# Kernel optimization log

Hardware: AMD Instinct MI355X
Metric: run time of the kernel (lower is better)

Reference implementation:

```python
import jax, jax.numpy as jnp
import numpy as np

N, E, D = 50000, 300000, 64
ETYPES = ['temporal', 'assigned_to', 'com', 'tin', 'win', 'sin', 'take_time', 'use_time']


def setup_inputs():
    key = jax.random.key(0)
    ks = iter(jax.random.split(key, 80))

    def nrm(shape, s=1.0):
        return jax.random.normal(next(ks), shape, dtype=jnp.float32) * s

    inp = {}
    inp['feat_task'] = nrm((N, D))
    inp['feat_worker'] = nrm((N, D))
    inp['feat_state'] = nrm((N, D))
    for et in ETYPES:
        inp['src_' + et] = jax.random.randint(next(ks), (E,), 0, N, dtype=jnp.int32)
        inp['dst_' + et] = jax.random.randint(next(ks), (E,), 0, N, dtype=jnp.int32)
    inp['w_temporal'] = jax.random.uniform(next(ks), (E, 1), dtype=jnp.float32)
    inp['t_take_time'] = jax.random.uniform(next(ks), (E, 1), dtype=jnp.float32)
    inp['t_use_time'] = jax.random.uniform(next(ks), (E, 1), dtype=jnp.float32)
    for et in ETYPES:
        inp['W_' + et] = nrm((D, D), 0.05)
        inp['b_' + et] = nrm((D,), 0.05)
    for nm in ['edge_fc', 'edge_fc_ttr', 'edge_fc_rut']:
        inp[nm + '_W'] = nrm((D, 1), 0.05)
        inp[nm + '_b'] = nrm((D,), 0.05)
    inp['attn_W'] = nrm((1, 3 * D), 0.05)
    inp['attn_ttr_W'] = nrm((1, 3 * D), 0.05)
    inp['attn_rut_W'] = nrm((1, 3 * D), 0.05)
    inp['attn_assigned_W'] = nrm((1, 2 * D), 0.05)
    inp['attn_com_W'] = nrm((1, 2 * D), 0.05)
    inp['attn_tin_W'] = nrm((1, 2 * D), 0.05)
    inp['attn_rin_W'] = nrm((1, 2 * D), 0.05)
    return inp


def _seg_softmax_sum(e, msg, dst, n):
    # numerically stable segment softmax over each dst node's incoming edges,
    # followed by the alpha-weighted scatter-sum (DGL reduce_func).
    m = jax.ops.segment_max(e, dst, num_segments=n)        # [n,1]
    ex = jnp.exp(e - m[dst])                               # [E,1]
    den = jax.ops.segment_sum(ex, dst, num_segments=n)     # [n,1]
    return jax.ops.segment_sum((ex / den[dst]) * msg, dst, num_segments=n)


def _gat(Wh_s, Wh_d, src, dst, aW, n, zij=None):
    # e = leaky_relu(attn_fc(concat(z_src, z_dst[, zij]))); the concat is never
    # materialized -- attn weight is split into per-block dot products.
    d = Wh_s.shape[1]
    zs = Wh_s[src]
    e = zs @ aW[0, :d] + Wh_d[dst] @ aW[0, d:2 * d]
    if zij is not None:
        e = e + zij @ aW[0, 2 * d:]
        msg = zs + zij   # message_func: src Wh + edge embedding
    else:
        msg = zs
    e = jax.nn.leaky_relu(e, 0.2)[:, None]
    return _seg_softmax_sum(e, msg, dst, n)


def _forward(feat_task, feat_worker, feat_state, w_temporal, t_take_time, t_use_time,
             W_temporal, b_temporal, W_assigned_to, b_assigned_to, W_com, b_com,
             W_tin, b_tin, W_win, b_win, W_sin, b_sin, W_take_time, b_take_time,
             W_use_time, b_use_time, edge_fc_W, edge_fc_b, edge_fc_ttr_W, edge_fc_ttr_b,
             edge_fc_rut_W, edge_fc_rut_b, attn_W, attn_assigned_W, attn_com_W,
             attn_tin_W, attn_rin_W, attn_ttr_W, attn_rut_W,
             src_temporal, dst_temporal, src_assigned_to, dst_assigned_to,
             src_com, dst_com, src_tin, dst_tin, src_win, dst_win,
             src_sin, dst_sin, src_take_time, dst_take_time, src_use_time, dst_use_time):
    n_task, n_worker, n_state = feat_task.shape[0], feat_worker.shape[0], feat_state.shape[0]
    # Equation (1): per-etype linear projection of source node features
    Wh_temporal = feat_task @ W_temporal.T + b_temporal
    Wh_assigned = feat_task @ W_assigned_to.T + b_assigned_to
    Wh_com = feat_worker @ W_com.T + b_com
    Wh_tin = feat_task @ W_tin.T + b_tin
    Wh_win = feat_worker @ W_win.T + b_win
    Wh_sin = feat_state @ W_sin.T + b_sin
    Wh_ttr = feat_task @ W_take_time.T + b_take_time
    Wh_rut = feat_worker @ W_use_time.T + b_use_time
    # per-edge scalar feature -> d-dim embedding
    zij_t = w_temporal @ edge_fc_W.T + edge_fc_b
    zij_ttr = t_take_time @ edge_fc_ttr_W.T + edge_fc_ttr_b
    zij_rut = t_use_time @ edge_fc_rut_W.T + edge_fc_rut_b
    # Equations (2)-(4): per-etype attention + segment softmax + scatter-sum
    h_temporal = _gat(Wh_temporal, Wh_temporal, src_temporal, dst_temporal, attn_W, n_task, zij_t)
    h_assigned = _gat(Wh_assigned, Wh_com, src_assigned_to, dst_assigned_to, attn_assigned_W, n_worker)
    h_com = _gat(Wh_com, Wh_com, src_com, dst_com, attn_com_W, n_worker)
    h_tin = _gat(Wh_tin, Wh_sin, src_tin, dst_tin, attn_tin_W, n_state)
    h_win = _gat(Wh_win, Wh_sin, src_win, dst_win, attn_rin_W, n_state)
    h_sin = jax.ops.segment_sum(Wh_sin[src_sin], dst_sin, num_segments=n_state)  # copy_src + sum
    h_ttr = _gat(Wh_ttr, Wh_com, src_take_time, dst_take_time, attn_ttr_W, n_worker, zij_ttr)
    h_rut = _gat(Wh_rut, Wh_temporal, src_use_time, dst_use_time, attn_rut_W, n_task, zij_rut)
    # multi_update_all cross-type 'sum', then ReLU
    h_task = jax.nn.relu(h_temporal + h_rut)
    h_worker = jax.nn.relu(h_assigned + h_com + h_ttr)
    h_state = jax.nn.relu(h_tin + h_win + h_sin)
    return jnp.stack([h_task, h_worker, h_state])  # [3, N, D]


def reference(feat_task, feat_worker, feat_state,
              src_temporal, dst_temporal, src_assigned_to, dst_assigned_to,
              src_com, dst_com, src_tin, dst_tin, src_win, dst_win,
              src_sin, dst_sin, src_take_time, dst_take_time, src_use_time, dst_use_time,
              w_temporal, t_take_time, t_use_time,
              W_temporal, b_temporal, W_assigned_to, b_assigned_to, W_com, b_com,
              W_tin, b_tin, W_win, b_win, W_sin, b_sin, W_take_time, b_take_time,
              W_use_time, b_use_time, edge_fc_W, edge_fc_b, edge_fc_ttr_W, edge_fc_ttr_b,
              edge_fc_rut_W, edge_fc_rut_b, attn_W, attn_ttr_W, attn_rut_W,
              attn_assigned_W, attn_com_W, attn_tin_W, attn_rin_W):
    return _forward(feat_task, feat_worker, feat_state, w_temporal, t_take_time, t_use_time,
                    W_temporal, b_temporal, W_assigned_to, b_assigned_to, W_com, b_com,
                    W_tin, b_tin, W_win, b_win, W_sin, b_sin, W_take_time, b_take_time,
                    W_use_time, b_use_time, edge_fc_W, edge_fc_b, edge_fc_ttr_W, edge_fc_ttr_b,
                    edge_fc_rut_W, edge_fc_rut_b, attn_W, attn_assigned_W, attn_com_W,
                    attn_tin_W, attn_rin_W, attn_ttr_W, attn_rut_W,
                    src_temporal, dst_temporal, src_assigned_to, dst_assigned_to,
                    src_com, dst_com, src_tin, dst_tin, src_win, dst_win,
                    src_sin, dst_sin, src_take_time, dst_take_time, src_use_time, dst_use_time)
```

## Files before the change

kernel.cpp:

```cpp
#include <hip/hip_runtime.h>
#include <math.h>

#define NN 50000
#define EE 300000
#define NG 8
#define NTOT (NG * NN)
#define NBKT 782
#define BCAP 3584
#define TILE 1024
#define NBLKE ((EE + TILE - 1) / TILE)

typedef unsigned short u16;
typedef unsigned int u32;
typedef short bf16x8 __attribute__((ext_vector_type(8)));
typedef float f32x16 __attribute__((ext_vector_type(16)));

__device__ __forceinline__ float b2f(u16 u) { return __uint_as_float(((u32)u) << 16); }
__device__ __forceinline__ u16 f2b(float f) {
    u32 x = __float_as_uint(f);
    u32 lsb = (x >> 16) & 1u;
    return (u16)((x + 0x7fffu + lsb) >> 16);
}

__global__ void HeteroGATLayer_14259291423309_kernel() {}

struct SetupP {
    int* gcur;
    const float* attn[3]; const float* fcW[3]; const float* fcb[3];
    float* consts;
};

__global__ __launch_bounds__(256) void k_setup(SetupP p) {
    const int i = blockIdx.x * 256 + threadIdx.x;
    if (i < NBKT) p.gcur[i] = 0;
    if (blockIdx.x == 3) {
        const int z = threadIdx.x >> 6, lane = threadIdx.x & 63;
        if (z < 3) {
            float a2 = p.attn[z][128 + lane];
            float x = p.fcW[z][lane] * a2;
            float y = p.fcb[z][lane] * a2;
            #pragma unroll
            for (int off = 32; off; off >>= 1) {
                x += __shfl_down(x, off);
                y += __shfl_down(y, off);
            }
            if (lane == 0) {
                const int co[3] = {0, 10, 12};
                p.consts[co[z]] = x;
                p.consts[co[z] + 1] = y;
            }
        }
    }
}

struct ProjP {
    const float* feat[3];
    const float* W[8]; const float* b[8];
    u16* wh;
    int ntile[3]; int tiles[3][4];
    int nvec[8];
    const float* avec[8][4];
    float* dvec[8][4];
};

__global__ __launch_bounds__(256) void k_proj(ProjP p) {
    __shared__ u16 sA[64 * 64];
    __shared__ u16 sW[64 * 64];
    __shared__ u16 sC[64 * 66];
    const int f = blockIdx.y;
    const int tid = threadIdx.x;
    const int row0 = blockIdx.x * 64;
    const float* feat = p.feat[f];

    #pragma unroll
    for (int q = 0; q < 4; ++q) {
        int idx = q * 256 + tid;
        int r = idx >> 4;
        int c4 = (idx & 15) * 4;
        int gr = row0 + r;
        if (gr >= NN) gr = NN - 1;
        float4 fv = *(const float4*)(feat + (size_t)gr * 64 + c4);
        *(ushort4*)&sA[r * 64 + c4] = make_ushort4(f2b(fv.x), f2b(fv.y), f2b(fv.z), f2b(fv.w));
    }

    const int wv = tid >> 6, lane = tid & 63;
    const int mrow = (wv & 1) * 32, ncol = (wv >> 1) * 32;
    const int half = lane >> 5, l31 = lane & 31;
    const int nt = p.ntile[f];

    for (int ti = 0; ti < nt; ++ti) {
        const int t = p.tiles[f][ti];
        const float* W = p.W[t];
        #pragma unroll
        for (int q = 0; q < 4; ++q) {
            int idx = q * 256 + tid;
            int r = idx >> 4;
            int c4 = (idx & 15) * 4;
            float4 wv4 = *(const float4*)(W + r * 64 + c4);
            *(ushort4*)&sW[r * 64 + c4] = make_ushort4(f2b(wv4.x), f2b(wv4.y), f2b(wv4.z), f2b(wv4.w));
        }
        __syncthreads();

        f32x16 acc;
        #pragma unroll
        for (int i = 0; i < 16; ++i) acc[i] = 0.0f;
        #pragma unroll
        for (int k0 = 0; k0 < 64; k0 += 16) {
            bf16x8 af = *(const bf16x8*)&sA[(mrow + l31) * 64 + k0 + half * 8];
            bf16x8 bf = *(const bf16x8*)&sW[(ncol + l31) * 64 + k0 + half * 8];
            acc = __builtin_amdgcn_mfma_f32_32x32x16_bf16(af, bf, acc, 0, 0, 0);
        }

        float bb = p.b[t][ncol + l31];
        u16* whp = p.wh + (size_t)t * NN * 64;
        #pragma unroll
        for (int reg = 0; reg < 16; ++reg) {
            int rowD = (reg & 3) + 8 * (reg >> 2) + 4 * half;
            int gr = row0 + mrow + rowD;
            u16 c16 = f2b(acc[reg] + bb);
            if (gr < NN) whp[(size_t)gr * 64 + ncol + l31] = c16;
            sC[(mrow + rowD) * 66 + ncol + l31] = c16;
        }
        __syncthreads();

        const int r = tid & 63, j = tid >> 6;
        if (j < p.nvec[t]) {
            const float* av = p.avec[t][j];
            float s = 0.f;
            #pragma unroll
            for (int c = 0; c < 64; c += 4) {
                ushort4 cv = *(const ushort4*)&sC[r * 66 + c];
                float4 a4 = *(const float4*)(av + c);
                s += b2f(cv.x) * a4.x + b2f(cv.y) * a4.y + b2f(cv.z) * a4.z + b2f(cv.w) * a4.w;
            }
            int gr = row0 + r;
            if (gr < NN) p.dvec[t][j][gr] = s;
        }
    }
}

struct BinAP {
    const int* src[8]; const int* dst[8]; const float* w[8];
    const float* el[8]; const float* er[8];
    const float* consts;
    int whoff[8];
    int* gcur; int4* bkt;
};

__global__ __launch_bounds__(256) void k_binA(BinAP p) {
    __shared__ int hist[128];
    const int g = blockIdx.y;
    const int b0 = (g * NN) >> 9;
    const int tid = threadIdx.x;
    const int e = blockIdx.x * TILE + tid * 4;
    if (tid < 128) hist[tid] = 0;

    const bool hw = p.w[g] != 0;
    float c1 = 0.f, c0 = 0.f;
    if (g < 7 && hw) { c1 = p.consts[2 * g]; c0 = p.consts[2 * g + 1]; }
    const int wo = p.whoff[g];

    int sr[4], bl[4], low[4];
    float sc[4], pw[4];
    const bool valid = e < EE;
    if (valid) {
        int4 s4 = *(const int4*)(p.src[g] + e);
        int4 d4 = *(const int4*)(p.dst[g] + e);
        float4 w4 = make_float4(0.f, 0.f, 0.f, 0.f);
        if (hw) w4 = *(const float4*)(p.w[g] + e);
        int ss[4] = {s4.x, s4.y, s4.z, s4.w};
        int dd[4] = {d4.x, d4.y, d4.z, d4.w};
        float ww[4] = {w4.x, w4.y, w4.z, w4.w};
        #pragma unroll
        for (int q = 0; q < 4; ++q) {
            int key = g * NN + dd[q];
            bl[q] = (key >> 9) - b0;
            low[q] = key & 511;
            sr[q] = wo + (ss[q] << 7);
            float scv = 1.0f, pwv = 0.0f;
            if (g < 7) {
                scv = p.el[g][ss[q]] + p.er[g][dd[q]];
                if (hw) scv += c1 * ww[q] + c0;
                scv = scv > 0.f ? scv : 0.2f * scv;
                scv = __expf(scv);
                if (hw) pwv = scv * ww[q];
            }
            sc[q] = scv; pw[q] = pwv;
        }
    }
    __syncthreads();
    if (valid) {
        #pragma unroll
        for (int q = 0; q < 4; ++q) atomicAdd(&hist[bl[q]], 1);
    }
    __syncthreads();
    if (tid < 128) {
        int c = hist[tid];
        hist[tid] = c ? atomicAdd(&p.gcur[b0 + tid], c) : 0;
    }
    __syncthreads();
    if (valid) {
        #pragma unroll
        for (int q = 0; q < 4; ++q) {
            int pos = atomicAdd(&hist[bl[q]], 1);
            int4 v;
            v.x = sr[q];
            v.y = __float_as_int(sc[q]);
            v.z = __float_as_int(pw[q]);
            v.w = low[q];
            p.bkt[(size_t)(b0 + bl[q]) * BCAP + pos] = v;
        }
    }
}

__global__ __launch_bounds__(512) void k_binB(const int* __restrict__ gcur,
                                              const int4* __restrict__ bkt,
                                              int2* __restrict__ csr,
                                              int4* __restrict__ rowdeg) {
    __shared__ int2 st2[BCAP];
    __shared__ float st3[BCAP];
    __shared__ int hist[512];
    __shared__ int scn[512];
    __shared__ int wsum[8];
    const int b = blockIdx.x;
    const int tid = threadIdx.x;
    int count = gcur[b];
    if (count > BCAP) count = BCAP;
    hist[tid] = 0;
    __syncthreads();
    const int4* src = bkt + (size_t)b * BCAP;
    for (int i = tid; i < count; i += 512) atomicAdd(&hist[src[i].w], 1);
    __syncthreads();
    int h = hist[tid];
    const int lane = tid & 63, wvi = tid >> 6;
    int incl = h;
    #pragma unroll
    for (int off = 1; off < 64; off <<= 1) {
        int t = __shfl_up(incl, off);
        if (lane >= off) incl += t;
    }
    if (lane == 63) wsum[wvi] = incl;
    __syncthreads();
    int wb = 0;
    #pragma unroll
    for (int w = 0; w < 8; ++w)
        if (w < wvi) wb += wsum[w];
    const int excl = wb + incl - h;
    scn[tid] = excl;
    __syncthreads();
    for (int i = tid; i < count; i += 512) {
        int4 v = src[i];
        int pos = atomicAdd(&scn[v.w], 1);
        st2[pos] = make_int2(v.x, v.y);
        st3[pos] = __int_as_float(v.z);
    }
    __syncthreads();
    float den = 0.f, sw = 0.f;
    for (int j = 0; j < h; ++j) {
        den += __int_as_float(st2[excl + j].y);
        sw += st3[excl + j];
    }
    const int gkey = b * 512 + tid;
    if (gkey < NTOT) {
        float inv = (gkey >= 7 * NN) ? 1.0f : ((h > 0 && den > 0.f) ? 1.0f / den : 0.f);
        u32 beg = (u32)(b * BCAP + excl);
        rowdeg[gkey] = make_int4((int)((beg << 10) | (u32)h),
                                 __float_as_int(inv), __float_as_int(sw * inv), 0);
    }
    for (int i = tid; i < count; i += 512) csr[(size_t)b * BCAP + i] = st2[i];
}

struct GathP {
    int gidx[3][3]; int hasfc[3][3];
    const float* fcW[3][3]; const float* fcb[3][3];
};

#define GSTEP4(t, sp)                                                              \
    {                                                                              \
        int2 e0 = sp[k], e1 = sp[k + 1], e2 = sp[k + 2], e3 = sp[k + 3];           \
        u32 w0 = *(const u32*)(whA + (u32)(e0.x + dby));                           \
        u32 w1 = *(const u32*)(whA + (u32)(e1.x + dby));                           \
        u32 w2 = *(const u32*)(whA + (u32)(e2.x + dby));                           \
        u32 w3 = *(const u32*)(whA + (u32)(e3.x + dby));                           \
        acc0[t] += __int_as_float(e0.y) * b2f((u16)w0);                            \
        acc1[t] += __int_as_float(e0.y) * b2f((u16)(w0 >> 16));                    \
        acc0[t] += __int_as_float(e1.y) * b2f((u16)w1);                            \
        acc1[t] += __int_as_float(e1.y) * b2f((u16)(w1 >> 16));                    \
        acc0[t] += __int_as_float(e2.y) * b2f((u16)w2);                            \
        acc1[t] += __int_as_float(e2.y) * b2f((u16)(w2 >> 16));                    \
        acc0[t] += __int_as_float(e3.y) * b2f((u16)w3);                            \
        acc1[t] += __int_as_float(e3.y) * b2f((u16)(w3 >> 16));                    \
    }

__global__ __launch_bounds__(256) void k_gather(GathP p,
        const int4* __restrict__ rowdeg, const int2* __restrict__ csr,
        const char* __restrict__ whA, float* __restrict__ out) {
    __shared__ int2 sSeg[4][3][2][64];
    const int tg = blockIdx.y;
    const int wv = threadIdx.x >> 6, lane = threadIdx.x & 63;
    const int half = lane >> 5, c = lane & 31;
    const int i = blockIdx.x * 8 + wv * 2 + half;
    const int dby = c * 4;
    const int ng = (tg == 0) ? 2 : 3;

    int lenv[3]; u32 begv[3]; float invv[3], swv[3];
    #pragma unroll
    for (int t = 0; t < 3; ++t) {
        lenv[t] = 0; begv[t] = 0; invv[t] = 0.f; swv[t] = 0.f;
        if (t < ng) {
            int4 rv = rowdeg[p.gidx[tg][t] * NN + i];
            lenv[t] = rv.x & 1023;
            begv[t] = ((u32)rv.x) >> 10;
            invv[t] = __int_as_float(rv.y);
            swv[t] = __int_as_float(rv.z);
        }
    }
    int lenA[3], lenB[3], lmax[3]; u32 begA[3], begB[3];
    #pragma unroll
    for (int t = 0; t < 3; ++t) {
        lenA[t] = __builtin_amdgcn_readlane(lenv[t], 0);
        lenB[t] = __builtin_amdgcn_readlane(lenv[t], 32);
        begA[t] = (u32)__builtin_amdgcn_readlane((int)begv[t], 0);
        begB[t] = (u32)__builtin_amdgcn_readlane((int)begv[t], 32);
        lmax[t] = lenA[t] > lenB[t] ? lenA[t] : lenB[t];
    }
    int kall = lmax[0] > lmax[1] ? lmax[0] : lmax[1];
    kall = kall > lmax[2] ? kall : lmax[2];

    float acc0[3] = {0.f, 0.f, 0.f}, acc1[3] = {0.f, 0.f, 0.f};
    for (int cb = 0; cb < kall; cb += 64) {
        #pragma unroll
        for (int t = 0; t < 3; ++t) {
            if (cb < lmax[t]) {
                int2 vA = (lane < lenA[t] - cb) ? csr[begA[t] + cb + lane] : make_int2(0, 0);
                sSeg[wv][t][0][lane] = vA;
                int2 vB = (lane < lenB[t] - cb) ? csr[begB[t] + cb + lane] : make_int2(0, 0);
                sSeg[wv][t][1][lane] = vB;
            }
        }
        const int2* s0 = sSeg[wv][0][half];
        const int2* s1 = sSeg[wv][1][half];
        const int2* s2 = sSeg[wv][2][half];
        int l0 = lmax[0] - cb, l1 = lmax[1] - cb, l2 = lmax[2] - cb;
        if (l0 > 64) l0 = 64;
        if (l1 > 64) l1 = 64;
        if (l2 > 64) l2 = 64;
        int cmax = l0 > l1 ? l0 : l1;
        cmax = cmax > l2 ? cmax : l2;
        for (int k = 0; k < cmax; k += 4) {
            if (k < l0) GSTEP4(0, s0)
            if (k < l1) GSTEP4(1, s1)
            if (k < l2) GSTEP4(2, s2)
        }
    }

    float tot0 = 0.f, tot1 = 0.f;
    #pragma unroll
    for (int t = 0; t < 3; ++t) {
        tot0 += acc0[t] * invv[t];
        tot1 += acc1[t] * invv[t];
        if (p.hasfc[tg][t]) {
            bool he = lenv[t] > 0;
            float2 fw = *(const float2*)(p.fcW[tg][t] + 2 * c);
            float2 fb = *(const float2*)(p.fcb[tg][t] + 2 * c);
            tot0 += he ? (fw.x * swv[t] + fb.x) : 0.f;
            tot1 += he ? (fw.y * swv[t] + fb.y) : 0.f;
        }
    }
    float2 o;
    o.x = tot0 > 0.f ? tot0 : 0.f;
    o.y = tot1 > 0.f ? tot1 : 0.f;
    *(float2*)(out + ((size_t)tg * NN + i) * 64 + 2 * c) = o;
}

extern "C" void kernel_launch(void* const* d_in, const int* in_sizes, int n_in,
                              void* d_out, int out_size, void* d_ws, size_t ws_size,
                              hipStream_t stream) {
    (void)in_sizes; (void)n_in; (void)out_size; (void)ws_size;
    const float* feats[3] = {(const float*)d_in[0], (const float*)d_in[1], (const float*)d_in[2]};
    const int* srcs[8];
    const int* dsts[8];
    for (int t = 0; t < 8; ++t) {
        srcs[t] = (const int*)d_in[3 + 2 * t];
        dsts[t] = (const int*)d_in[4 + 2 * t];
    }
    const float* ew0 = (const float*)d_in[19];
    const float* ew1 = (const float*)d_in[20];
    const float* ew2 = (const float*)d_in[21];
    const float* Wm[8];
    const float* bm[8];
    for (int t = 0; t < 8; ++t) {
        Wm[t] = (const float*)d_in[22 + 2 * t];
        bm[t] = (const float*)d_in[23 + 2 * t];
    }
    const float* fcW0 = (const float*)d_in[38];
    const float* fcb0 = (const float*)d_in[39];
    const float* fcW1 = (const float*)d_in[40];
    const float* fcb1 = (const float*)d_in[41];
    const float* fcW2 = (const float*)d_in[42];
    const float* fcb2 = (const float*)d_in[43];
    const float* attn_W          = (const float*)d_in[44];
    const float* attn_ttr_W      = (const float*)d_in[45];
    const float* attn_rut_W      = (const float*)d_in[46];
    const float* attn_assigned_W = (const float*)d_in[47];
    const float* attn_com_W      = (const float*)d_in[48];
    const float* attn_tin_W      = (const float*)d_in[49];
    const float* attn_rin_W      = (const float*)d_in[50];

    u16* Wh = (u16*)d_ws;
    char* b0 = (char*)d_ws + (size_t)8 * NN * 64 * sizeof(u16);
    float* el     = (float*)b0;
    float* er     = el + (size_t)7 * NN;
    float* consts = er + (size_t)7 * NN;
    int* gcur     = (int*)(consts + 16);
    int4* rowdeg4 = (int4*)(((size_t)(gcur + NBKT) + 15) & ~(size_t)15);
    int4* bkt     = rowdeg4 + NTOT;
    int2* csr     = (int2*)(bkt + (size_t)NBKT * BCAP);

    int g_et[8]   = {0, 1, 2, 3, 4, 6, 7, 5};
    int g_sidx[8] = {0, 1, 2, 3, 4, 6, 7, 5};
    const float* g_w[8] = {ew0, 0, 0, 0, 0, ew1, ew2, 0};

    {
        SetupP sp;
        sp.gcur = gcur;
        sp.attn[0] = attn_W;     sp.fcW[0] = fcW0; sp.fcb[0] = fcb0;
        sp.attn[1] = attn_ttr_W; sp.fcW[1] = fcW1; sp.fcb[1] = fcb1;
        sp.attn[2] = attn_rut_W; sp.fcW[2] = fcW2; sp.fcb[2] = fcb2;
        sp.consts = consts;
        k_setup<<<4, 256, 0, stream>>>(sp);
    }

    {
        ProjP pp;
        pp.feat[0] = feats[0]; pp.feat[1] = feats[1]; pp.feat[2] = feats[2];
        for (int t = 0; t < 8; ++t) { pp.W[t] = Wm[t]; pp.b[t] = bm[t]; }
        pp.wh = Wh;
        pp.ntile[0] = 4; pp.tiles[0][0] = 0; pp.tiles[0][1] = 1; pp.tiles[0][2] = 3; pp.tiles[0][3] = 6;
        pp.ntile[1] = 3; pp.tiles[1][0] = 2; pp.tiles[1][1] = 4; pp.tiles[1][2] = 7; pp.tiles[1][3] = 0;
        pp.ntile[2] = 1; pp.tiles[2][0] = 5; pp.tiles[2][1] = 0; pp.tiles[2][2] = 0; pp.tiles[2][3] = 0;
        for (int t = 0; t < 8; ++t) {
            pp.nvec[t] = 0;
            for (int j = 0; j < 4; ++j) { pp.avec[t][j] = 0; pp.dvec[t][j] = 0; }
        }
        auto setv = [&](int t, int j, const float* a, float* dv) { pp.avec[t][j] = a; pp.dvec[t][j] = dv; };
        pp.nvec[0] = 3; setv(0, 0, attn_W, el);           setv(0, 1, attn_W + 64, er);
                        setv(0, 2, attn_rut_W + 64, er + 6 * NN);
        pp.nvec[1] = 1; setv(1, 0, attn_assigned_W, el + 1 * NN);
        pp.nvec[2] = 4; setv(2, 0, attn_com_W, el + 2 * NN); setv(2, 1, attn_assigned_W + 64, er + 1 * NN);
                        setv(2, 2, attn_com_W + 64, er + 2 * NN); setv(2, 3, attn_ttr_W + 64, er + 5 * NN);
        pp.nvec[3] = 1; setv(3, 0, attn_tin_W, el + 3 * NN);
        pp.nvec[4] = 1; setv(4, 0, attn_rin_W, el + 4 * NN);
        pp.nvec[5] = 2; setv(5, 0, attn_tin_W + 64, er + 3 * NN); setv(5, 1, attn_rin_W + 64, er + 4 * NN);
        pp.nvec[6] = 1; setv(6, 0, attn_ttr_W, el + 5 * NN);
        pp.nvec[7] = 1; setv(7, 0, attn_rut_W, el + 6 * NN);
        k_proj<<<dim3(782, 3), 256, 0, stream>>>(pp);
    }

    {
        BinAP bp;
        for (int g = 0; g < 8; ++g) {
            bp.src[g] = srcs[g_et[g]];
            bp.dst[g] = dsts[g_et[g]];
            bp.w[g] = g_w[g];
            bp.el[g] = (g < 7) ? el + (size_t)g * NN : 0;
            bp.er[g] = (g < 7) ? er + (size_t)g * NN : 0;
            bp.whoff[g] = g_sidx[g] * NN * 128;
        }
        bp.consts = consts;
        bp.gcur = gcur;
        bp.bkt = bkt;
        k_binA<<<dim3(NBLKE, 8), 256, 0, stream>>>(bp);
    }
    k_binB<<<NBKT, 512, 0, stream>>>(gcur, bkt, csr, rowdeg4);

    {
        GathP gp;
        gp.gidx[0][0] = 0; gp.hasfc[0][0] = 1; gp.fcW[0][0] = fcW0; gp.fcb[0][0] = fcb0;
        gp.gidx[0][1] = 6; gp.hasfc[0][1] = 1; gp.fcW[0][1] = fcW2; gp.fcb[0][1] = fcb2;
        gp.gidx[0][2] = 0; gp.hasfc[0][2] = 0; gp.fcW[0][2] = fcW0; gp.fcb[0][2] = fcb0;
        gp.gidx[1][0] = 1; gp.hasfc[1][0] = 0; gp.fcW[1][0] = fcW0; gp.fcb[1][0] = fcb0;
        gp.gidx[1][1] = 2; gp.hasfc[1][1] = 0; gp.fcW[1][1] = fcW0; gp.fcb[1][1] = fcb0;
        gp.gidx[1][2] = 5; gp.hasfc[1][2] = 1; gp.fcW[1][2] = fcW1; gp.fcb[1][2] = fcb1;
        gp.gidx[2][0] = 3; gp.hasfc[2][0] = 0; gp.fcW[2][0] = fcW0; gp.fcb[2][0] = fcb0;
        gp.gidx[2][1] = 4; gp.hasfc[2][1] = 0; gp.fcW[2][1] = fcW0; gp.fcb[2][1] = fcb0;
        gp.gidx[2][2] = 7; gp.hasfc[2][2] = 0; gp.fcW[2][2] = fcW0; gp.fcb[2][2] = fcb0;
        k_gather<<<dim3(NN / 8, 3), 256, 0, stream>>>(gp, rowdeg4, csr,
                                                      (const char*)Wh, (float*)d_out);
    }
}
```

Baseline: 345.9 us.

## Fuse bucket sort and gather into per-node-block kernel with all types bucketed together

Edges of all eight relation types are now bucketed by destination node block (64 nodes × 8 types per bucket) in one binning launch, instead of one bucket range per type. A single fused kernel then sorts each bucket in shared memory, normalizes the softmax weights in place, and directly gathers the projected features and writes outputs for all three node types. This removes the separate CSR and rowdeg write-out, the extra kernel launch, and the reread of CSR from global memory. In exchange, bucket capacity per block must hold all types' edges, and each block's gather now loops over 64 nodes with a load-imbalanced inner loop.

```diff
diff --git a/kernel.cpp b/kernel.cpp
--- a/kernel.cpp
+++ b/kernel.cpp
@@ -4,7 +4,6 @@
 #define NN 50000
 #define EE 300000
 #define NG 8
-#define NTOT (NG * NN)
 #define NBKT 782
 #define BCAP 3584
 #define TILE 1024
@@ -45,7 +44,7 @@
                 y += __shfl_down(y, off);
             }
             if (lane == 0) {
-                const int co[3] = {0, 10, 12};
+                const int co[3] = {0, 8, 2};
                 p.consts[co[z]] = x;
                 p.consts[co[z] + 1] = y;
             }
@@ -147,80 +146,98 @@
     int* gcur; int4* bkt;
 };
 
-__global__ __launch_bounds__(256) void k_binA(BinAP p) {
-    __shared__ int hist[128];
-    const int g = blockIdx.y;
-    const int b0 = (g * NN) >> 9;
+__global__ __launch_bounds__(512) void k_binA(BinAP p) {
+    __shared__ int hist[784];
     const int tid = threadIdx.x;
-    const int e = blockIdx.x * TILE + tid * 4;
-    if (tid < 128) hist[tid] = 0;
-
-    const bool hw = p.w[g] != 0;
-    float c1 = 0.f, c0 = 0.f;
-    if (g < 7 && hw) { c1 = p.consts[2 * g]; c0 = p.consts[2 * g + 1]; }
-    const int wo = p.whoff[g];
-
-    int sr[4], bl[4], low[4];
-    float sc[4], pw[4];
+    const int e = blockIdx.x * TILE + tid * 2;
+    for (int i = tid; i < 784; i += 512) hist[i] = 0;
     const bool valid = e < EE;
-    if (valid) {
-        int4 s4 = *(const int4*)(p.src[g] + e);
-        int4 d4 = *(const int4*)(p.dst[g] + e);
-        float4 w4 = make_float4(0.f, 0.f, 0.f, 0.f);
-        if (hw) w4 = *(const float4*)(p.w[g] + e);
-        int ss[4] = {s4.x, s4.y, s4.z, s4.w};
-        int dd[4] = {d4.x, d4.y, d4.z, d4.w};
-        float ww[4] = {w4.x, w4.y, w4.z, w4.w};
+    int d0[8], d1[8];
+    __syncthreads();
+    #pragma unroll
+    for (int g = 0; g < 8; ++g) {
+        int2 dv = valid ? *(const int2*)(p.dst[g] + e) : make_int2(0, 0);
+        d0[g] = dv.x; d1[g] = dv.y;
+        if (valid) {
+            atomicAdd(&hist[dv.x >> 6], 1);
+            atomicAdd(&hist[dv.y >> 6], 1);
+        }
+    }
+    __syncthreads();
+    for (int b = tid; b < NBKT; b += 512) {
+        int c = hist[b];
+        hist[b] = c ? atomicAdd(&p.gcur[b], c) : 0;
+    }
+    __syncthreads();
+    #pragma unroll
+    for (int g = 0; g < 8; ++g) {
+        if (!valid) continue;
+        int2 sv = *(const int2*)(p.src[g] + e);
+        const float* wp = p.w[g];
+        const bool hw = wp != 0;
+        float2 wv = hw ? *(const float2*)(wp + e) : make_float2(0.f, 0.f);
+        float c1 = 0.f, c0 = 0.f;
+        if (g < 7 && hw) { c1 = p.consts[2 * g]; c0 = p.consts[2 * g + 1]; }
+        const int wo = p.whoff[g];
+        int ss[2] = {sv.x, sv.y};
+        int dd[2] = {d0[g], d1[g]};
+        float ww[2] = {wv.x, wv.y};
         #pragma unroll
-        for (int q = 0; q < 4; ++q) {
-            int key = g * NN + dd[q];
-            bl[q] = (key >> 9) - b0;
-            low[q] = key & 511;
-            sr[q] = wo + (ss[q] << 7);
-            float scv = 1.0f, pwv = 0.0f;
+        for (int q = 0; q < 2; ++q) {
+            float sc = 1.0f, pw = 0.0f;
             if (g < 7) {
-                scv = p.el[g][ss[q]] + p.er[g][dd[q]];
-                if (hw) scv += c1 * ww[q] + c0;
-                scv = scv > 0.f ? scv : 0.2f * scv;
-                scv = __expf(scv);
-                if (hw) pwv = scv * ww[q];
+                sc = p.el[g][ss[q]] + p.er[g][dd[q]];
+                if (hw) sc += c1 * ww[q] + c0;
+                sc = sc > 0.f ? sc : 0.2f * sc;
+                sc = __expf(sc);
+                if (hw) pw = sc * ww[q];
             }
-            sc[q] = scv; pw[q] = pwv;
-        }
-    }
-    __syncthreads();
-    if (valid) {
-        #pragma unroll
-        for (int q = 0; q < 4; ++q) atomicAdd(&hist[bl[q]], 1);
-    }
-    __syncthreads();
-    if (tid < 128) {
-        int c = hist[tid];
-        hist[tid] = c ? atomicAdd(&p.gcur[b0 + tid], c) : 0;
-    }
-    __syncthreads();
-    if (valid) {
-        #pragma unroll
-        for (int q = 0; q < 4; ++q) {
-            int pos = atomicAdd(&hist[bl[q]], 1);
+            int bkt_i = dd[q] >> 6;
+            int pos = atomicAdd(&hist[bkt_i], 1);
             int4 v;
-            v.x = sr[q];
-            v.y = __float_as_int(sc[q]);
-            v.z = __float_as_int(pw[q]);
-            v.w = low[q];
-            p.bkt[(size_t)(b0 + bl[q]) * BCAP + pos] = v;
-        }
-    }
-}
-
-__global__ __launch_bounds__(512) void k_binB(const int* __restrict__ gcur,
-                                              const int4* __restrict__ bkt,
-                                              int2* __restrict__ csr,
-                                              int4* __restrict__ rowdeg) {
-    __shared__ int2 st2[BCAP];
+            v.x = wo + (ss[q] << 7);
+            v.y = __float_as_int(sc);
+            v.z = __float_as_int(pw);
+            v.w = ((dd[q] & 63) << 3) | g;
+            p.bkt[(size_t)bkt_i * BCAP + pos] = v;
+        }
+    }
+}
+
+struct BgP {
+    const float* fcW[3]; const float* fcb[3];
+};
+
+#define BGSTEP4(t, baseV, lenV)                                                    \
+    {                                                                              \
+        int2 e0 = st2[baseV + k], e1 = st2[baseV + k + 1];                         \
+        int2 e2 = st2[baseV + k + 2], e3 = st2[baseV + k + 3];                     \
+        int o0 = (k < lenV) ? e0.x : 0;                                            \
+        int o1 = (k + 1 < lenV) ? e1.x : 0;                                        \
+        int o2 = (k + 2 < lenV) ? e2.x : 0;                                        \
+        int o3 = (k + 3 < lenV) ? e3.x : 0;                                        \
+        float f0 = (k < lenV) ? __int_as_float(e0.y) : 0.f;                        \
+        float f1 = (k + 1 < lenV) ? __int_as_float(e1.y) : 0.f;                    \
+        float f2 = (k + 2 < lenV) ? __int_as_float(e2.y) : 0.f;                    \
+        float f3 = (k + 3 < lenV) ? __int_as_float(e3.y) : 0.f;                    \
+        u32 w0 = *(const u32*)(whA + (u32)(o0 + dby));                             \
+        u32 w1 = *(const u32*)(whA + (u32)(o1 + dby));                             \
+        u32 w2 = *(const u32*)(whA + (u32)(o2 + dby));                             \
+        u32 w3 = *(const u32*)(whA + (u32)(o3 + dby));                             \
+        a0[t] += f0 * b2f((u16)w0); a1[t] += f0 * b2f((u16)(w0 >> 16));            \
+        a0[t] += f1 * b2f((u16)w1); a1[t] += f1 * b2f((u16)(w1 >> 16));            \
+        a0[t] += f2 * b2f((u16)w2); a1[t] += f2 * b2f((u16)(w2 >> 16));            \
+        a0[t] += f3 * b2f((u16)w3); a1[t] += f3 * b2f((u16)(w3 >> 16));            \
+    }
+
+__global__ __launch_bounds__(512) void k_bg(BgP p, const int* __restrict__ gcur,
+        const int4* __restrict__ bkt, const char* __restrict__ whA,
+        float* __restrict__ out) {
+    __shared__ int2 st2[BCAP + 128];
     __shared__ float st3[BCAP];
     __shared__ int hist[512];
     __shared__ int scn[512];
+    __shared__ float sSw[512];
     __shared__ int wsum[8];
     const int b = blockIdx.x;
     const int tid = threadIdx.x;
@@ -260,117 +277,71 @@
         den += __int_as_float(st2[excl + j].y);
         sw += st3[excl + j];
     }
-    const int gkey = b * 512 + tid;
-    if (gkey < NTOT) {
-        float inv = (gkey >= 7 * NN) ? 1.0f : ((h > 0 && den > 0.f) ? 1.0f / den : 0.f);
-        u32 beg = (u32)(b * BCAP + excl);
-        rowdeg[gkey] = make_int4((int)((beg << 10) | (u32)h),
-                                 __float_as_int(inv), __float_as_int(sw * inv), 0);
-    }
-    for (int i = tid; i < count; i += 512) csr[(size_t)b * BCAP + i] = st2[i];
-}
-
-struct GathP {
-    int gidx[3][3]; int hasfc[3][3];
-    const float* fcW[3][3]; const float* fcb[3][3];
-};
-
-#define GSTEP4(t, sp)                                                              \
-    {                                                                              \
-        int2 e0 = sp[k], e1 = sp[k + 1], e2 = sp[k + 2], e3 = sp[k + 3];           \
-        u32 w0 = *(const u32*)(whA + (u32)(e0.x + dby));                           \
-        u32 w1 = *(const u32*)(whA + (u32)(e1.x + dby));                           \
-        u32 w2 = *(const u32*)(whA + (u32)(e2.x + dby));                           \
-        u32 w3 = *(const u32*)(whA + (u32)(e3.x + dby));                           \
-        acc0[t] += __int_as_float(e0.y) * b2f((u16)w0);                            \
-        acc1[t] += __int_as_float(e0.y) * b2f((u16)(w0 >> 16));                    \
-        acc0[t] += __int_as_float(e1.y) * b2f((u16)w1);                            \
-        acc1[t] += __int_as_float(e1.y) * b2f((u16)(w1 >> 16));                    \
-        acc0[t] += __int_as_float(e2.y) * b2f((u16)w2);                            \
-        acc1[t] += __int_as_float(e2.y) * b2f((u16)(w2 >> 16));                    \
-        acc0[t] += __int_as_float(e3.y) * b2f((u16)w3);                            \
-        acc1[t] += __int_as_float(e3.y) * b2f((u16)(w3 >> 16));                    \
-    }
-
-__global__ __launch_bounds__(256) void k_gather(GathP p,
-        const int4* __restrict__ rowdeg, const int2* __restrict__ csr,
-        const char* __restrict__ whA, float* __restrict__ out) {
-    __shared__ int2 sSeg[4][3][2][64];
-    const int tg = blockIdx.y;
-    const int wv = threadIdx.x >> 6, lane = threadIdx.x & 63;
+    const int gk = tid & 7;
+    float inv = (gk == 7) ? 1.0f : ((h > 0 && den > 0.f) ? 1.0f / den : 0.f);
+    sSw[tid] = sw * inv;
+    for (int j = 0; j < h; ++j)
+        st2[excl + j].y = __float_as_int(__int_as_float(st2[excl + j].y) * inv);
+    __syncthreads();
     const int half = lane >> 5, c = lane & 31;
-    const int i = blockIdx.x * 8 + wv * 2 + half;
     const int dby = c * 4;
-    const int ng = (tg == 0) ? 2 : 3;
-
-    int lenv[3]; u32 begv[3]; float invv[3], swv[3];
-    #pragma unroll
-    for (int t = 0; t < 3; ++t) {
-        lenv[t] = 0; begv[t] = 0; invv[t] = 0.f; swv[t] = 0.f;
-        if (t < ng) {
-            int4 rv = rowdeg[p.gidx[tg][t] * NN + i];
-            lenv[t] = rv.x & 1023;
-            begv[t] = ((u32)rv.x) >> 10;
-            invv[t] = __int_as_float(rv.y);
-            swv[t] = __int_as_float(rv.z);
-        }
-    }
-    int lenA[3], lenB[3], lmax[3]; u32 begA[3], begB[3];
-    #pragma unroll
-    for (int t = 0; t < 3; ++t) {
-        lenA[t] = __builtin_amdgcn_readlane(lenv[t], 0);
-        lenB[t] = __builtin_amdgcn_readlane(lenv[t], 32);
-        begA[t] = (u32)__builtin_amdgcn_readlane((int)begv[t], 0);
-        begB[t] = (u32)__builtin_amdgcn_readlane((int)begv[t], 32);
-        lmax[t] = lenA[t] > lenB[t] ? lenA[t] : lenB[t];
-    }
-    int kall = lmax[0] > lmax[1] ? lmax[0] : lmax[1];
-    kall = kall > lmax[2] ? kall : lmax[2];
-
-    float acc0[3] = {0.f, 0.f, 0.f}, acc1[3] = {0.f, 0.f, 0.f};
-    for (int cb = 0; cb < kall; cb += 64) {
-        #pragma unroll
-        for (int t = 0; t < 3; ++t) {
-            if (cb < lmax[t]) {
-                int2 vA = (lane < lenA[t] - cb) ? csr[begA[t] + cb + lane] : make_int2(0, 0);
-                sSeg[wv][t][0][lane] = vA;
-                int2 vB = (lane < lenB[t] - cb) ? csr[begB[t] + cb + lane] : make_int2(0, 0);
-                sSeg[wv][t][1][lane] = vB;
-            }
-        }
-        const int2* s0 = sSeg[wv][0][half];
-        const int2* s1 = sSeg[wv][1][half];
-        const int2* s2 = sSeg[wv][2][half];
-        int l0 = lmax[0] - cb, l1 = lmax[1] - cb, l2 = lmax[2] - cb;
-        if (l0 > 64) l0 = 64;
-        if (l1 > 64) l1 = 64;
-        if (l2 > 64) l2 = 64;
-        int cmax = l0 > l1 ? l0 : l1;
-        cmax = cmax > l2 ? cmax : l2;
-        for (int k = 0; k < cmax; k += 4) {
-            if (k < l0) GSTEP4(0, s0)
-            if (k < l1) GSTEP4(1, s1)
-            if (k < l2) GSTEP4(2, s2)
-        }
-    }
-
-    float tot0 = 0.f, tot1 = 0.f;
-    #pragma unroll
-    for (int t = 0; t < 3; ++t) {
-        tot0 += acc0[t] * invv[t];
-        tot1 += acc1[t] * invv[t];
-        if (p.hasfc[tg][t]) {
-            bool he = lenv[t] > 0;
-            float2 fw = *(const float2*)(p.fcW[tg][t] + 2 * c);
-            float2 fb = *(const float2*)(p.fcb[tg][t] + 2 * c);
-            tot0 += he ? (fw.x * swv[t] + fb.x) : 0.f;
-            tot1 += he ? (fw.y * swv[t] + fb.y) : 0.f;
-        }
-    }
-    float2 o;
-    o.x = tot0 > 0.f ? tot0 : 0.f;
-    o.y = tot1 > 0.f ? tot1 : 0.f;
-    *(float2*)(out + ((size_t)tg * NN + i) * 64 + 2 * c) = o;
+    for (int pass = 0; pass < 4; ++pass) {
+        const int nl = pass * 16 + wvi * 2 + half;
+        const int n8 = nl * 8;
+        int bT = scn[n8] - hist[n8];
+        int eT = scn[n8 + 1];
+        int eW = scn[n8 + 4];
+        int eS = scn[n8 + 7];
+        int lT = eT - bT, lW = eW - eT, lS = eS - eW;
+        int lTa = __builtin_amdgcn_readlane(lT, 0), lTb = __builtin_amdgcn_readlane(lT, 32);
+        int lWa = __builtin_amdgcn_readlane(lW, 0), lWb = __builtin_amdgcn_readlane(lW, 32);
+        int lSa = __builtin_amdgcn_readlane(lS, 0), lSb = __builtin_amdgcn_readlane(lS, 32);
+        int lTm = lTa > lTb ? lTa : lTb;
+        int lWm = lWa > lWb ? lWa : lWb;
+        int lSm = lSa > lSb ? lSa : lSb;
+        int kmax = lTm > lWm ? lTm : lWm;
+        kmax = kmax > lSm ? kmax : lSm;
+
+        float a0[3] = {0.f, 0.f, 0.f}, a1[3] = {0.f, 0.f, 0.f};
+        for (int k = 0; k < kmax; k += 4) {
+            if (k < lTm) BGSTEP4(0, bT, lT)
+            if (k < lWm) BGSTEP4(1, eT, lW)
+            if (k < lSm) BGSTEP4(2, eW, lS)
+        }
+
+        float tT0 = a0[0], tT1 = a1[0];
+        if (hist[n8] > 0) {
+            float2 fw = *(const float2*)(p.fcW[0] + 2 * c);
+            float2 fb = *(const float2*)(p.fcb[0] + 2 * c);
+            float s = sSw[n8];
+            tT0 += fw.x * s + fb.x; tT1 += fw.y * s + fb.y;
+        }
+        if (hist[n8 + 1] > 0) {
+            float2 fw = *(const float2*)(p.fcW[2] + 2 * c);
+            float2 fb = *(const float2*)(p.fcb[2] + 2 * c);
+            float s = sSw[n8 + 1];
+            tT0 += fw.x * s + fb.x; tT1 += fw.y * s + fb.y;
+        }
+        float tW0 = a0[1], tW1 = a1[1];
+        if (hist[n8 + 4] > 0) {
+            float2 fw = *(const float2*)(p.fcW[1] + 2 * c);
+            float2 fb = *(const float2*)(p.fcb[1] + 2 * c);
+            float s = sSw[n8 + 4];
+            tW0 += fw.x * s + fb.x; tW1 += fw.y * s + fb.y;
+        }
+        float tS0 = a0[2], tS1 = a1[2];
+
+        const int gnode = b * 64 + nl;
+        if (gnode < NN) {
+            float2 o;
+            o.x = tT0 > 0.f ? tT0 : 0.f; o.y = tT1 > 0.f ? tT1 : 0.f;
+            *(float2*)(out + ((size_t)0 * NN + gnode) * 64 + 2 * c) = o;
+            o.x = tW0 > 0.f ? tW0 : 0.f; o.y = tW1 > 0.f ? tW1 : 0.f;
+            *(float2*)(out + ((size_t)1 * NN + gnode) * 64 + 2 * c) = o;
+            o.x = tS0 > 0.f ? tS0 : 0.f; o.y = tS1 > 0.f ? tS1 : 0.f;
+            *(float2*)(out + ((size_t)2 * NN + gnode) * 64 + 2 * c) = o;
+        }
+    }
 }
 
 extern "C" void kernel_launch(void* const* d_in, const int* in_sizes, int n_in,
@@ -413,13 +384,11 @@
     float* er     = el + (size_t)7 * NN;
     float* consts = er + (size_t)7 * NN;
     int* gcur     = (int*)(consts + 16);
-    int4* rowdeg4 = (int4*)(((size_t)(gcur + NBKT) + 15) & ~(size_t)15);
-    int4* bkt     = rowdeg4 + NTOT;
-    int2* csr     = (int2*)(bkt + (size_t)NBKT * BCAP);
-
-    int g_et[8]   = {0, 1, 2, 3, 4, 6, 7, 5};
-    int g_sidx[8] = {0, 1, 2, 3, 4, 6, 7, 5};
-    const float* g_w[8] = {ew0, 0, 0, 0, 0, ew1, ew2, 0};
+    int4* bkt     = (int4*)(((size_t)(gcur + NBKT) + 15) & ~(size_t)15);
+
+    int g_et[8]   = {0, 7, 1, 2, 6, 3, 4, 5};
+    int g_sidx[8] = {0, 7, 1, 2, 6, 3, 4, 5};
+    const float* g_w[8] = {ew0, ew2, 0, 0, ew1, 0, 0, 0};
 
     {
         SetupP sp;
@@ -444,16 +413,20 @@
             for (int j = 0; j < 4; ++j) { pp.avec[t][j] = 0; pp.dvec[t][j] = 0; }
         }
         auto setv = [&](int t, int j, const float* a, float* dv) { pp.avec[t][j] = a; pp.dvec[t][j] = dv; };
-        pp.nvec[0] = 3; setv(0, 0, attn_W, el);           setv(0, 1, attn_W + 64, er);
-                        setv(0, 2, attn_rut_W + 64, er + 6 * NN);
-        pp.nvec[1] = 1; setv(1, 0, attn_assigned_W, el + 1 * NN);
-        pp.nvec[2] = 4; setv(2, 0, attn_com_W, el + 2 * NN); setv(2, 1, attn_assigned_W + 64, er + 1 * NN);
-                        setv(2, 2, attn_com_W + 64, er + 2 * NN); setv(2, 3, attn_ttr_W + 64, er + 5 * NN);
-        pp.nvec[3] = 1; setv(3, 0, attn_tin_W, el + 3 * NN);
-        pp.nvec[4] = 1; setv(4, 0, attn_rin_W, el + 4 * NN);
-        pp.nvec[5] = 2; setv(5, 0, attn_tin_W + 64, er + 3 * NN); setv(5, 1, attn_rin_W + 64, er + 4 * NN);
-        pp.nvec[6] = 1; setv(6, 0, attn_ttr_W, el + 5 * NN);
-        pp.nvec[7] = 1; setv(7, 0, attn_rut_W, el + 6 * NN);
+        pp.nvec[0] = 3; setv(0, 0, attn_W, el + 0 * NN);
+                        setv(0, 1, attn_W + 64, er + 0 * NN);
+                        setv(0, 2, attn_rut_W + 64, er + 1 * NN);
+        pp.nvec[1] = 1; setv(1, 0, attn_assigned_W, el + 2 * NN);
+        pp.nvec[2] = 4; setv(2, 0, attn_com_W, el + 3 * NN);
+                        setv(2, 1, attn_assigned_W + 64, er + 2 * NN);
+                        setv(2, 2, attn_com_W + 64, er + 3 * NN);
+                        setv(2, 3, attn_ttr_W + 64, er + 4 * NN);
+        pp.nvec[3] = 1; setv(3, 0, attn_tin_W, el + 5 * NN);
+        pp.nvec[4] = 1; setv(4, 0, attn_rin_W, el + 6 * NN);
+        pp.nvec[5] = 2; setv(5, 0, attn_tin_W + 64, er + 5 * NN);
+                        setv(5, 1, attn_rin_W + 64, er + 6 * NN);
+        pp.nvec[6] = 1; setv(6, 0, attn_ttr_W, el + 4 * NN);
+        pp.nvec[7] = 1; setv(7, 0, attn_rut_W, el + 1 * NN);
         k_proj<<<dim3(782, 3), 256, 0, stream>>>(pp);
     }
 
@@ -470,22 +443,14 @@
         bp.consts = consts;
         bp.gcur = gcur;
         bp.bkt = bkt;
-        k_binA<<<dim3(NBLKE, 8), 256, 0, stream>>>(bp);
-    }
-    k_binB<<<NBKT, 512, 0, stream>>>(gcur, bkt, csr, rowdeg4);
+        k_binA<<<NBLKE, 512, 0, stream>>>(bp);
+    }
 
     {
-        GathP gp;
-        gp.gidx[0][0] = 0; gp.hasfc[0][0] = 1; gp.fcW[0][0] = fcW0; gp.fcb[0][0] = fcb0;
-        gp.gidx[0][1] = 6; gp.hasfc[0][1] = 1; gp.fcW[0][1] = fcW2; gp.fcb[0][1] = fcb2;
-        gp.gidx[0][2] = 0; gp.hasfc[0][2] = 0; gp.fcW[0][2] = fcW0; gp.fcb[0][2] = fcb0;
-        gp.gidx[1][0] = 1; gp.hasfc[1][0] = 0; gp.fcW[1][0] = fcW0; gp.fcb[1][0] = fcb0;
-        gp.gidx[1][1] = 2; gp.hasfc[1][1] = 0; gp.fcW[1][1] = fcW0; gp.fcb[1][1] = fcb0;
-        gp.gidx[1][2] = 5; gp.hasfc[1][2] = 1; gp.fcW[1][2] = fcW1; gp.fcb[1][2] = fcb1;
-        gp.gidx[2][0] = 3; gp.hasfc[2][0] = 0; gp.fcW[2][0] = fcW0; gp.fcb[2][0] = fcb0;
-        gp.gidx[2][1] = 4; gp.hasfc[2][1] = 0; gp.fcW[2][1] = fcW0; gp.fcb[2][1] = fcb0;
-        gp.gidx[2][2] = 7; gp.hasfc[2][2] = 0; gp.fcW[2][2] = fcW0; gp.fcb[2][2] = fcb0;
-        k_gather<<<dim3(NN / 8, 3), 256, 0, stream>>>(gp, rowdeg4, csr,
-                                                      (const char*)Wh, (float*)d_out);
-    }
-}
+        BgP gp;
+        gp.fcW[0] = fcW0; gp.fcb[0] = fcb0;
+        gp.fcW[1] = fcW1; gp.fcb[1] = fcb1;
+        gp.fcW[2] = fcW2; gp.fcb[2] = fcb2;
+        k_bg<<<NBKT, 512, 0, stream>>>(gp, gcur, bkt, (const char*)Wh, (float*)d_out);
+    }
+}
```

After: 388.7 us. 12.4% more time.
